# Kernel optimization log

Hardware: AMD Instinct MI355X
Metric: run time of the kernel (lower is better)

Reference implementation:

```python
import jax, jax.numpy as jnp
import numpy as np

DIM = 1024
NUM_HEADS = 16
HEAD_DIM = DIM // NUM_HEADS
WINDOW = 16
B, S = 2, 8192
MAX_POS = 8192


def setup_inputs() -> dict:
    key = jax.random.key(0)
    ks = jax.random.split(key, 6)
    x = jax.random.normal(ks[0], (B, S, DIM), dtype=jnp.float32)
    # rope angle table [max_pos, head_dim//2]
    rope_freqs = jax.random.uniform(ks[1], (MAX_POS, HEAD_DIM // 2), dtype=jnp.float32)
    scale = 1.0 / np.sqrt(DIM)
    wq = jax.random.normal(ks[2], (DIM, DIM), dtype=jnp.float32) * scale
    wk = jax.random.normal(ks[3], (DIM, DIM), dtype=jnp.float32) * scale
    wv = jax.random.normal(ks[4], (DIM, DIM), dtype=jnp.float32) * scale
    wo = jax.random.normal(ks[5], (DIM, DIM), dtype=jnp.float32) * scale
    return {"x": x, "rope_freqs": rope_freqs, "wq": wq, "wk": wk, "wv": wv, "wo": wo}


def _apply_rope(t, cos, sin):
    # t: [N, W, H, hd]; cos/sin: [1, W, 1, hd//2] (split-half rotation)
    t1, t2 = jnp.split(t, 2, axis=-1)
    return jnp.concatenate([t1 * cos - t2 * sin, t1 * sin + t2 * cos], axis=-1)


def reference(x, rope_freqs, wq, wk, wv, wo):
    Bx, Sx, D = x.shape
    W, H, hd = WINDOW, NUM_HEADS, HEAD_DIM
    n_windows = Sx // W  # S chosen divisible by W (pad = 0 path)
    xw = x.reshape(Bx * n_windows, W, D)
    q = (xw @ wq.T).reshape(Bx * n_windows, W, H, hd)
    k = (xw @ wk.T).reshape(Bx * n_windows, W, H, hd)
    v = (xw @ wv.T).reshape(Bx * n_windows, W, H, hd)
    # position_ids=None path: positions are arange(W) in every window
    freqs = rope_freqs[jnp.arange(W)]                 # [W, hd//2]
    cos = jnp.cos(freqs)[None, :, None, :]
    sin = jnp.sin(freqs)[None, :, None, :]
    q = _apply_rope(q, cos, sin)
    k = _apply_rope(k, cos, sin)
    # non-causal flash attention within each window
    scores = jnp.einsum('nqhd,nkhd->nhqk', q, k) / jnp.sqrt(jnp.float32(hd))
    probs = jax.nn.softmax(scores, axis=-1)
    attn = jnp.einsum('nhqk,nkhd->nqhd', probs, v)    # [B*nw, W, H, hd]
    attn = attn.reshape(Bx, Sx, H * hd)
    return attn @ wo.T
```

## Files before the change

### kernel.cpp

```cpp
#include <hip/hip_runtime.h>
#include <hip/hip_bf16.h>
#include <stdint.h>

typedef short bf16x8 __attribute__((ext_vector_type(8)));
typedef short bf16x4 __attribute__((ext_vector_type(4)));
typedef float f32x4  __attribute__((ext_vector_type(4)));

__device__ __forceinline__ float b2f(short s) {
  union { float f; uint32_t u; } x;
  x.u = ((uint32_t)(uint16_t)s) << 16;
  return x.f;
}
__device__ __forceinline__ short f2b(float f) {
  union { float f; uint32_t u; } x;
  x.f = f;
  uint32_t r = x.u + 0x7fff + ((x.u >> 16) & 1);
  return (short)(r >> 16);
}

__device__ __forceinline__ void gload_lds16(const void* g, void* l) {
  __builtin_amdgcn_global_load_lds(
      (const __attribute__((address_space(1))) void*)g,
      (__attribute__((address_space(3))) void*)l, 16, 0, 0);
}

__global__ __launch_bounds__(256)
void prep(const float* __restrict__ x, const float* __restrict__ rope,
          const float* __restrict__ wq, const float* __restrict__ wk,
          const float* __restrict__ wv, const float* __restrict__ wo,
          short* __restrict__ Xb, short* __restrict__ Wqkv, short* __restrict__ Wob,
          float* __restrict__ costab, float* __restrict__ sintab)
{
  const int64_t XN4 = 16777216 / 4;
  const int64_t WN4 = 1048576 / 4;
  const int64_t total = XN4 + 4 * WN4 + 512;
  for (int64_t i = (int64_t)blockIdx.x * blockDim.x + threadIdx.x; i < total;
       i += (int64_t)gridDim.x * blockDim.x) {
    if (i < XN4) {
      f32x4 v = ((const f32x4*)x)[i];
      bf16x4 o;
#pragma unroll
      for (int j = 0; j < 4; ++j) o[j] = f2b(v[j]);
      ((bf16x4*)Xb)[i] = o;
    } else if (i < XN4 + 3 * WN4) {
      int64_t j = i - XN4;
      const float* src = (j < WN4) ? wq : ((j < 2 * WN4) ? wk : wv);
      int64_t jj = j & (WN4 - 1);
      f32x4 v = ((const f32x4*)src)[jj];
      bf16x4 o;
#pragma unroll
      for (int q = 0; q < 4; ++q) o[q] = f2b(v[q]);
      ((bf16x4*)Wqkv)[j] = o;
    } else if (i < XN4 + 4 * WN4) {
      int64_t j = i - XN4 - 3 * WN4;
      f32x4 v = ((const f32x4*)wo)[j];
      bf16x4 o;
#pragma unroll
      for (int q = 0; q < 4; ++q) o[q] = f2b(v[q]);
      ((bf16x4*)Wob)[j] = o;
    } else {
      int64_t j = i - XN4 - 4 * WN4;
      int pos = (int)(j >> 5), f = (int)(j & 31);
      float a = rope[pos * 32 + f];
      costab[j] = cosf(a);
      sintab[j] = sinf(a);
    }
  }
}

__device__ __forceinline__ void store4(short* C, size_t idx, f32x4 v) {
  bf16x4 o;
#pragma unroll
  for (int j = 0; j < 4; ++j) o[j] = f2b(v[j]);
  *(bf16x4*)(C + idx) = o;
}
__device__ __forceinline__ void store4(float* C, size_t idx, f32x4 v) {
  *(f32x4*)(C + idx) = v;
}

template <typename OutT>
__global__ __launch_bounds__(512, 2)
void gemm_bt2(const short* __restrict__ A, const short* __restrict__ Bw,
              OutT* __restrict__ C, int M, int N, int K, int nmt)
{
  __shared__ __align__(16) char lds[147456];
  const int t = threadIdx.x;
  const int lane = t & 63;
  const int wid = t >> 6;
  const int wm = wid >> 2;
  const int wn = wid & 3;

  int nwg = gridDim.x;
  int bid = blockIdx.x;
  int swz = ((nwg & 7) == 0) ? ((bid & 7) * (nwg >> 3) + (bid >> 3)) : bid;
  const int mt = swz % nmt;
  const int nt = swz / nmt;
  const int m0 = mt << 7;
  const int n0 = nt << 8;

  const int T = K >> 6;

  const int r_a  = lane >> 3;
  const int csrc = lane & 7;

  auto stageA = [&](int kt, int buf) {
    char* base = lds + buf * 49152;
#pragma unroll
    for (int j = 0; j < 2; ++j) {
      int chunk = j * 8 + wid;
      int r = chunk * 8 + r_a;
      int sl = csrc ^ (r & 7);
      gload_lds16(A + (size_t)(m0 + r) * K + (kt << 6) + (sl << 3),
                  base + chunk * 1024);
    }
  };
  auto stageB = [&](int kt, int buf) {
    char* base = lds + buf * 49152 + 16384;
#pragma unroll
    for (int j = 0; j < 4; ++j) {
      int chunk = j * 8 + wid;
      int r = chunk * 8 + r_a;
      int sl = csrc ^ (r & 7);
      gload_lds16(Bw + (size_t)(n0 + r) * K + (kt << 6) + (sl << 3),
                  base + chunk * 1024);
    }
  };

  f32x4 acc[4][4];
#pragma unroll
  for (int m = 0; m < 4; ++m)
#pragma unroll
    for (int n = 0; n < 4; ++n) acc[m][n] = (f32x4){0.f, 0.f, 0.f, 0.f};

  const int lr = lane & 15;
  const int ls = lane >> 4;
  const int axor = lr & 7;

  stageA(0, 0); stageB(0, 0);
  if (T > 1) { stageA(1, 1); stageB(1, 1); }

  for (int kt = 0; kt < T; ++kt) {
    if (kt + 1 < T) asm volatile("s_waitcnt vmcnt(6)" ::: "memory");
    else            asm volatile("s_waitcnt vmcnt(0)" ::: "memory");
    __builtin_amdgcn_s_barrier();
    __builtin_amdgcn_sched_barrier(0);

    const int buf = kt % 3;
    if (kt + 2 < T) { const int nb = (kt + 2) % 3; stageA(kt + 2, nb); stageB(kt + 2, nb); }

    const char* ab = lds + buf * 49152;
    const char* bb = ab + 16384;
    bf16x8 af[2][4], bfr[2][4];
#pragma unroll
    for (int kk = 0; kk < 2; ++kk) {
      const int u = (((kk << 2) + ls) ^ axor) << 4;
#pragma unroll
      for (int m4 = 0; m4 < 4; ++m4)
        af[kk][m4] = *(const bf16x8*)(ab + (wm * 64 + m4 * 16 + lr) * 128 + u);
#pragma unroll
      for (int n4 = 0; n4 < 4; ++n4)
        bfr[kk][n4] = *(const bf16x8*)(bb + (wn * 64 + n4 * 16 + lr) * 128 + u);
    }

    __builtin_amdgcn_s_setprio(1);
#pragma unroll
    for (int kk = 0; kk < 2; ++kk)
#pragma unroll
      for (int m4 = 0; m4 < 4; ++m4)
#pragma unroll
        for (int n4 = 0; n4 < 4; ++n4)
          acc[m4][n4] = __builtin_amdgcn_mfma_f32_16x16x32_bf16(
              bfr[kk][n4], af[kk][m4], acc[m4][n4], 0, 0, 0);
    __builtin_amdgcn_s_setprio(0);
  }

  const int orow = m0 + wm * 64 + lr;
  const int ocol = n0 + wn * 64 + ls * 4;
#pragma unroll
  for (int m4 = 0; m4 < 4; ++m4)
#pragma unroll
    for (int n4 = 0; n4 < 4; ++n4)
      store4(C, (size_t)(orow + m4 * 16) * N + (ocol + n4 * 16), acc[m4][n4]);
}

__global__ __launch_bounds__(256)
void attn_win(const short* __restrict__ QKV,
              const float* __restrict__ costab, const float* __restrict__ sintab,
              short* __restrict__ Attn)
{
  __shared__ float Plds[4][16][17];
  __shared__ short Vlds[4][16][64];
  const int t = threadIdx.x, lane = t & 63, wid = t >> 6;
  const int pair = blockIdx.x * 4 + wid;
  const int win = pair >> 4, h = pair & 15;
  const int lr = lane & 15;
  const int lk = (lane >> 4) << 3;

  const size_t rowb = (size_t)(win * 16 + lr) * 3072;
  const short* qp = QKV + rowb + h * 64;
  const short* kp = qp + 1024;

  bf16x8 q0 = *(const bf16x8*)(qp + lk);
  bf16x8 q1 = *(const bf16x8*)(qp + 32 + lk);
  bf16x8 k0 = *(const bf16x8*)(kp + lk);
  bf16x8 k1 = *(const bf16x8*)(kp + 32 + lk);

#pragma unroll
  for (int j = 0; j < 2; ++j) {
    int e = (j * 64 + lane) * 8;
    int vr = e >> 6, vc = e & 63;
    *(bf16x8*)&Vlds[wid][vr][vc] =
        *(const bf16x8*)(QKV + (size_t)(win * 16 + vr) * 3072 + 2048 + h * 64 + vc);
  }

  bf16x8 a0, a1, b0, b1;
#pragma unroll
  for (int j = 0; j < 8; ++j) {
    int f = lk + j;
    float c = costab[lr * 32 + f], s = sintab[lr * 32 + f];
    float x1 = b2f(q0[j]), x2 = b2f(q1[j]);
    a0[j] = f2b(x1 * c - x2 * s);
    a1[j] = f2b(x1 * s + x2 * c);
    float y1 = b2f(k0[j]), y2 = b2f(k1[j]);
    b0[j] = f2b(y1 * c - y2 * s);
    b1[j] = f2b(y1 * s + y2 * c);
  }

  f32x4 sc = (f32x4){0.f, 0.f, 0.f, 0.f};
  sc = __builtin_amdgcn_mfma_f32_16x16x32_bf16(a0, b0, sc, 0, 0, 0);
  sc = __builtin_amdgcn_mfma_f32_16x16x32_bf16(a1, b1, sc, 0, 0, 0);

  float p[4];
#pragma unroll
  for (int i = 0; i < 4; ++i) {
    float v = sc[i] * 0.125f;
    float m = v;
#pragma unroll
    for (int msk = 1; msk < 16; msk <<= 1) m = fmaxf(m, __shfl_xor(m, msk));
    float e = __expf(v - m);
    float s = e;
#pragma unroll
    for (int msk = 1; msk < 16; msk <<= 1) s += __shfl_xor(s, msk);
    p[i] = e / s;
  }
#pragma unroll
  for (int i = 0; i < 4; ++i)
    Plds[wid][((lane >> 4) << 2) + i][lr] = p[i];

  __syncthreads();

  const int r = lr, dblk = lane >> 4;
  float a[16];
#pragma unroll
  for (int j = 0; j < 16; ++j) a[j] = 0.f;
#pragma unroll
  for (int k = 0; k < 16; ++k) {
    float pk = Plds[wid][r][k];
    bf16x8 v0 = *(const bf16x8*)&Vlds[wid][k][dblk * 16];
    bf16x8 v1 = *(const bf16x8*)&Vlds[wid][k][dblk * 16 + 8];
#pragma unroll
    for (int j = 0; j < 8; ++j) {
      a[j]     += pk * b2f(v0[j]);
      a[8 + j] += pk * b2f(v1[j]);
    }
  }
  bf16x8 o0, o1;
#pragma unroll
  for (int j = 0; j < 8; ++j) { o0[j] = f2b(a[j]); o1[j] = f2b(a[8 + j]); }
  short* op = Attn + (size_t)(win * 16 + r) * 1024 + h * 64 + dblk * 16;
  *(bf16x8*)op = o0;
  *(bf16x8*)(op + 8) = o1;
}

extern "C" void kernel_launch(void* const* d_in, const int* in_sizes, int n_in,
                              void* d_out, int out_size, void* d_ws, size_t ws_size,
                              hipStream_t stream)
{
  const float* x  = (const float*)d_in[0];
  const float* rf = (const float*)d_in[1];
  const float* wq = (const float*)d_in[2];
  const float* wk = (const float*)d_in[3];
  const float* wv = (const float*)d_in[4];
  const float* wo = (const float*)d_in[5];
  float* out = (float*)d_out;

  char* w = (char*)d_ws;
  short* Xb     = (short*)(w);
  short* Wqkv   = (short*)(w + 33554432);
  short* Wob    = (short*)(w + 39845888);
  short* QKV    = (short*)(w + 41943040);
  short* Attn   = (short*)(w + 142606336);
  float* costab = (float*)(w + 176160768);
  float* sintab = (float*)(w + 176162816);

  prep<<<2048, 256, 0, stream>>>(x, rf, wq, wk, wv, wo, Xb, Wqkv, Wob, costab, sintab);
  gemm_bt2<short><<<1536, 512, 0, stream>>>(Xb, Wqkv, QKV, 16384, 3072, 1024, 128);
  attn_win<<<4096, 256, 0, stream>>>(QKV, costab, sintab, Attn);
  gemm_bt2<float><<<512, 512, 0, stream>>>(Attn, Wob, out, 16384, 1024, 1024, 128);
}
```

Baseline: 353.8 us.

## Enlarge GEMM tiles to 256x256 with quadrant-interleaved double-buffered pipeline

Replaces the 128x256 triple-buffered GEMM with a 256x256 tile where each wave computes a 128x64 sub-block in four quadrant phases. Global-to-LDS loads for the next K step are interleaved between MFMA quadrants with double buffering. The goal is higher arithmetic intensity per LDS byte and better overlap of loads with MFMA. The cost is more accumulator registers (128 floats), many extra barriers, fewer workgroups (768 and 256), and a risk of wave-quantization imbalance on the output GEMM.

```diff
diff --git a/kernel.cpp b/kernel.cpp
--- a/kernel.cpp
+++ b/kernel.cpp
@@ -80,104 +80,129 @@
 
 template <typename OutT>
 __global__ __launch_bounds__(512, 2)
-void gemm_bt2(const short* __restrict__ A, const short* __restrict__ Bw,
+void gemm_bt3(const short* __restrict__ A, const short* __restrict__ Bw,
               OutT* __restrict__ C, int M, int N, int K, int nmt)
 {
-  __shared__ __align__(16) char lds[147456];
-  const int t = threadIdx.x;
-  const int lane = t & 63;
-  const int wid = t >> 6;
-  const int wm = wid >> 2;
-  const int wn = wid & 3;
-
-  int nwg = gridDim.x;
-  int bid = blockIdx.x;
-  int swz = ((nwg & 7) == 0) ? ((bid & 7) * (nwg >> 3) + (bid >> 3)) : bid;
-  const int mt = swz % nmt;
-  const int nt = swz / nmt;
-  const int m0 = mt << 7;
-  const int n0 = nt << 8;
-
+  __shared__ __align__(16) char lds[131072];
+  const int t = threadIdx.x, lane = t & 63, wid = t >> 6;
+  const int wm = wid >> 2, wn = wid & 3;
+  const int lr = lane & 15, ls = lane >> 4;
+
+  const int nwg = gridDim.x, bid = blockIdx.x;
+  const int swz = (bid & 7) * (nwg >> 3) + (bid >> 3);
+  const int mt = swz % nmt, nt = swz / nmt;
+  const int m0 = mt << 8, n0 = nt << 8;
   const int T = K >> 6;
 
-  const int r_a  = lane >> 3;
-  const int csrc = lane & 7;
-
-  auto stageA = [&](int kt, int buf) {
-    char* base = lds + buf * 49152;
+  const int srow8 = lane >> 3;
+  const int sgr   = (lane & 7) ^ srow8;
+
+  auto stageA = [&](int kt, int rh) {
+    char* base = lds + (kt & 1) * 65536;
 #pragma unroll
     for (int j = 0; j < 2; ++j) {
-      int chunk = j * 8 + wid;
-      int r = chunk * 8 + r_a;
-      int sl = csrc ^ (r & 7);
-      gload_lds16(A + (size_t)(m0 + r) * K + (kt << 6) + (sl << 3),
-                  base + chunk * 1024);
+      int c  = j * 8 + wid;
+      int rb = (c >> 3) * 128 + rh * 64 + (c & 7) * 8;
+      gload_lds16(A + (size_t)(m0 + rb + srow8) * K + (kt << 6) + (sgr << 3),
+                  base + rb * 128);
     }
   };
-  auto stageB = [&](int kt, int buf) {
-    char* base = lds + buf * 49152 + 16384;
-#pragma unroll
-    for (int j = 0; j < 4; ++j) {
-      int chunk = j * 8 + wid;
-      int r = chunk * 8 + r_a;
-      int sl = csrc ^ (r & 7);
-      gload_lds16(Bw + (size_t)(n0 + r) * K + (kt << 6) + (sl << 3),
-                  base + chunk * 1024);
+  auto stageB = [&](int kt, int ch) {
+    char* base = lds + (kt & 1) * 65536 + 32768;
+#pragma unroll
+    for (int j = 0; j < 2; ++j) {
+      int c  = j * 8 + wid;
+      int rb = (c >> 2) * 64 + ch * 32 + (c & 3) * 8;
+      gload_lds16(Bw + (size_t)(n0 + rb + srow8) * K + (kt << 6) + (sgr << 3),
+                  base + rb * 128);
     }
   };
 
-  f32x4 acc[4][4];
-#pragma unroll
-  for (int m = 0; m < 4; ++m)
+  f32x4 acc[8][4];
+#pragma unroll
+  for (int m = 0; m < 8; ++m)
 #pragma unroll
     for (int n = 0; n < 4; ++n) acc[m][n] = (f32x4){0.f, 0.f, 0.f, 0.f};
 
-  const int lr = lane & 15;
-  const int ls = lane >> 4;
-  const int axor = lr & 7;
-
-  stageA(0, 0); stageB(0, 0);
-  if (T > 1) { stageA(1, 1); stageB(1, 1); }
+  bf16x8 a[2][4], b[2][2];
+  auto ldA = [&](int kt, int rh) {
+    const char* base = lds + (kt & 1) * 65536;
+#pragma unroll
+    for (int kk = 0; kk < 2; ++kk)
+#pragma unroll
+      for (int i = 0; i < 4; ++i) {
+        int row = wm * 128 + (rh * 4 + i) * 16 + lr;
+        int u = ((kk << 2) + ls) ^ (lr & 7);
+        a[kk][i] = *(const bf16x8*)(base + row * 128 + u * 16);
+      }
+  };
+  auto ldB = [&](int kt, int ch) {
+    const char* base = lds + (kt & 1) * 65536 + 32768;
+#pragma unroll
+    for (int kk = 0; kk < 2; ++kk)
+#pragma unroll
+      for (int j = 0; j < 2; ++j) {
+        int row = wn * 64 + (ch * 2 + j) * 16 + lr;
+        int u = ((kk << 2) + ls) ^ (lr & 7);
+        b[kk][j] = *(const bf16x8*)(base + row * 128 + u * 16);
+      }
+  };
+  auto mfma16 = [&](int rh, int ch) {
+    __builtin_amdgcn_s_setprio(1);
+#pragma unroll
+    for (int kk = 0; kk < 2; ++kk)
+#pragma unroll
+      for (int i = 0; i < 4; ++i)
+#pragma unroll
+        for (int j = 0; j < 2; ++j)
+          acc[rh * 4 + i][ch * 2 + j] = __builtin_amdgcn_mfma_f32_16x16x32_bf16(
+              b[kk][j], a[kk][i], acc[rh * 4 + i][ch * 2 + j], 0, 0, 0);
+    __builtin_amdgcn_s_setprio(0);
+  };
+
+  stageA(0, 0); stageB(0, 0); stageB(0, 1); stageA(0, 1);
+  asm volatile("s_waitcnt vmcnt(4)" ::: "memory");
+  __builtin_amdgcn_s_barrier();
 
   for (int kt = 0; kt < T; ++kt) {
-    if (kt + 1 < T) asm volatile("s_waitcnt vmcnt(6)" ::: "memory");
-    else            asm volatile("s_waitcnt vmcnt(0)" ::: "memory");
-    __builtin_amdgcn_s_barrier();
+    const bool pf = (kt + 1 < T);
+    ldA(kt, 0); ldB(kt, 0);
+    if (pf) { stageA(kt + 1, 0); asm volatile("s_waitcnt vmcnt(4)" ::: "memory"); }
+    else    {                    asm volatile("s_waitcnt vmcnt(2)" ::: "memory"); }
+    asm volatile("s_waitcnt lgkmcnt(8)" ::: "memory");
+    __builtin_amdgcn_s_barrier();
+    asm volatile("s_waitcnt lgkmcnt(0)" ::: "memory");
     __builtin_amdgcn_sched_barrier(0);
-
-    const int buf = kt % 3;
-    if (kt + 2 < T) { const int nb = (kt + 2) % 3; stageA(kt + 2, nb); stageB(kt + 2, nb); }
-
-    const char* ab = lds + buf * 49152;
-    const char* bb = ab + 16384;
-    bf16x8 af[2][4], bfr[2][4];
-#pragma unroll
-    for (int kk = 0; kk < 2; ++kk) {
-      const int u = (((kk << 2) + ls) ^ axor) << 4;
-#pragma unroll
-      for (int m4 = 0; m4 < 4; ++m4)
-        af[kk][m4] = *(const bf16x8*)(ab + (wm * 64 + m4 * 16 + lr) * 128 + u);
-#pragma unroll
-      for (int n4 = 0; n4 < 4; ++n4)
-        bfr[kk][n4] = *(const bf16x8*)(bb + (wn * 64 + n4 * 16 + lr) * 128 + u);
-    }
-
-    __builtin_amdgcn_s_setprio(1);
-#pragma unroll
-    for (int kk = 0; kk < 2; ++kk)
-#pragma unroll
-      for (int m4 = 0; m4 < 4; ++m4)
-#pragma unroll
-        for (int n4 = 0; n4 < 4; ++n4)
-          acc[m4][n4] = __builtin_amdgcn_mfma_f32_16x16x32_bf16(
-              bfr[kk][n4], af[kk][m4], acc[m4][n4], 0, 0, 0);
-    __builtin_amdgcn_s_setprio(0);
-  }
-
-  const int orow = m0 + wm * 64 + lr;
+    mfma16(0, 0);
+    __builtin_amdgcn_s_barrier();
+    ldB(kt, 1);
+    if (pf) { stageB(kt + 1, 0); asm volatile("s_waitcnt vmcnt(4)" ::: "memory"); }
+    else    {                    asm volatile("s_waitcnt vmcnt(0)" ::: "memory"); }
+    __builtin_amdgcn_s_barrier();
+    asm volatile("s_waitcnt lgkmcnt(0)" ::: "memory");
+    __builtin_amdgcn_sched_barrier(0);
+    mfma16(0, 1);
+    __builtin_amdgcn_s_barrier();
+    ldA(kt, 1);
+    if (pf) stageB(kt + 1, 1);
+    __builtin_amdgcn_s_barrier();
+    asm volatile("s_waitcnt lgkmcnt(0)" ::: "memory");
+    __builtin_amdgcn_sched_barrier(0);
+    mfma16(1, 1);
+    __builtin_amdgcn_s_barrier();
+    ldB(kt, 0);
+    if (pf) { stageA(kt + 1, 1); asm volatile("s_waitcnt vmcnt(4)" ::: "memory"); }
+    __builtin_amdgcn_s_barrier();
+    asm volatile("s_waitcnt lgkmcnt(0)" ::: "memory");
+    __builtin_amdgcn_sched_barrier(0);
+    mfma16(1, 0);
+    __builtin_amdgcn_s_barrier();
+  }
+
+  const int orow = m0 + wm * 128 + lr;
   const int ocol = n0 + wn * 64 + ls * 4;
 #pragma unroll
-  for (int m4 = 0; m4 < 4; ++m4)
+  for (int m4 = 0; m4 < 8; ++m4)
 #pragma unroll
     for (int n4 = 0; n4 < 4; ++n4)
       store4(C, (size_t)(orow + m4 * 16) * N + (ocol + n4 * 16), acc[m4][n4]);
@@ -294,7 +319,7 @@
   float* sintab = (float*)(w + 176162816);
 
   prep<<<2048, 256, 0, stream>>>(x, rf, wq, wk, wv, wo, Xb, Wqkv, Wob, costab, sintab);
-  gemm_bt2<short><<<1536, 512, 0, stream>>>(Xb, Wqkv, QKV, 16384, 3072, 1024, 128);
+  gemm_bt3<short><<<768, 512, 0, stream>>>(Xb, Wqkv, QKV, 16384, 3072, 1024, 64);
   attn_win<<<4096, 256, 0, stream>>>(QKV, costab, sintab, Attn);
-  gemm_bt2<float><<<512, 512, 0, stream>>>(Attn, Wob, out, 16384, 1024, 1024, 128);
-}
+  gemm_bt3<float><<<256, 512, 0, stream>>>(Attn, Wob, out, 16384, 1024, 1024, 64);
+}
```

Result: faster. 332.2 us (-6.1%).
